# Kernel optimization log

Measured on AMD Instinct MI355X. Metric: run time of the kernel, lower is better.

## Reference

```python
import jax, jax.numpy as jnp
import numpy as np

B, T, V, D, H = 64, 256, 16, 64, 256  # batch, time, n_vars, d_inp, hidden


def setup_inputs() -> dict:
    key = jax.random.key(0)
    ks = jax.random.split(key, 20)
    s = 0.02
    inp = {
        "x": jax.random.normal(ks[0], (B, T, V, D), dtype=jnp.float32),
        # weight GRN: inp = V*D, hidden = H, out = V (skip linear present since V*D != V)
        "w_fc1_w": jax.random.normal(ks[1], (V * D, H), jnp.float32) * s,
        "w_fc1_b": jnp.zeros((H,), jnp.float32),
        "w_fc2_w": jax.random.normal(ks[2], (H, V), jnp.float32) * s,
        "w_fc2_b": jnp.zeros((V,), jnp.float32),
        "w_gate_w": jax.random.normal(ks[3], (V, V), jnp.float32) * s,
        "w_gate_b": jnp.zeros((V,), jnp.float32),
        "w_skip_w": jax.random.normal(ks[4], (V * D, V), jnp.float32) * s,
        "w_skip_b": jnp.zeros((V,), jnp.float32),
        # per-variable GRNs stacked over V: inp = D, hidden = H, out = H (skip since D != H)
        "v_fc1_w": jax.random.normal(ks[5], (V, D, H), jnp.float32) * s,
        "v_fc1_b": jnp.zeros((V, H), jnp.float32),
        "v_fc2_w": jax.random.normal(ks[6], (V, H, H), jnp.float32) * s,
        "v_fc2_b": jnp.zeros((V, H), jnp.float32),
        "v_gate_w": jax.random.normal(ks[7], (V, H, H), jnp.float32) * s,
        "v_gate_b": jnp.zeros((V, H), jnp.float32),
        "v_skip_w": jax.random.normal(ks[8], (V, D, H), jnp.float32) * s,
        "v_skip_b": jnp.zeros((V, H), jnp.float32),
    }
    return inp


def reference(x, w_fc1_w, w_fc1_b, w_fc2_w, w_fc2_b, w_gate_w, w_gate_b,
              w_skip_w, w_skip_b, v_fc1_w, v_fc1_b, v_fc2_w, v_fc2_b,
              v_gate_w, v_gate_b, v_skip_w, v_skip_b):
    # dropout is identity at inference
    Bx, Tx, Vx, Dx = x.shape
    flat = x.reshape(Bx, Tx, Vx * Dx)  # [B,T,V*D]

    # --- weight GRN: (V*D) -> V ---
    h = jax.nn.elu(flat @ w_fc1_w + w_fc1_b)          # [B,T,H]
    y = h @ w_fc2_w + w_fc2_b                          # [B,T,V]
    gate = jax.nn.sigmoid(y @ w_gate_w + w_gate_b)     # [B,T,V]
    res = flat @ w_skip_w + w_skip_b                   # [B,T,V]
    w = jax.nn.softmax(res + gate * y, axis=-1)        # [B,T,V]

    # --- per-variable GRNs, batched over V: D -> H ---
    hv = jax.nn.elu(jnp.einsum('btvd,vdh->btvh', x, v_fc1_w) + v_fc1_b)        # [B,T,V,H]
    yv = jnp.einsum('btvh,vhk->btvk', hv, v_fc2_w) + v_fc2_b                   # [B,T,V,H]
    gv = jax.nn.sigmoid(jnp.einsum('btvk,vkm->btvm', yv, v_gate_w) + v_gate_b) # [B,T,V,H]
    rv = jnp.einsum('btvd,vdk->btvk', x, v_skip_w) + v_skip_b                  # [B,T,V,H]
    var_outs = rv + gv * yv                                                    # [B,T,V,H]

    # softmax-weighted sum over variables
    z = jnp.einsum('btv,btvh->bth', w, var_outs)       # [B,T,H]
    return z
```

## Files before the change

### kernel.cpp

```cpp
#include <hip/hip_runtime.h>

typedef unsigned short u16;
typedef unsigned int   u32;
typedef __bf16 bf16x8 __attribute__((ext_vector_type(8)));
typedef u16    u16x8  __attribute__((ext_vector_type(8)));
typedef float  f32x4  __attribute__((ext_vector_type(4)));

#define DI static __device__ __forceinline__

DI float b2f(u16 u){ union { u32 i; float f; } c; c.i = ((u32)u) << 16; return c.f; }
DI u16 f2b(float f){ union { float f; u32 i; } c; c.f = f; u32 i = c.i;
                     return (u16)((i + 0x7FFFu + ((i >> 16) & 1u)) >> 16); }
DI float eluf(float x){ return x > 0.f ? x : (__expf(x) - 1.f); }
DI float sigf(float x){ return 1.f / (1.f + __expf(-x)); }
DI f32x4 mfma16(bf16x8 a, bf16x8 b, f32x4 c){
  return __builtin_amdgcn_mfma_f32_16x16x32_bf16(a, b, c, 0, 0, 0);
}
DI bf16x8 ldb(const u16* p){ return *(const bf16x8*)p; }

__global__ __launch_bounds__(256) void k_pack_x(
    const float* __restrict__ x, u16* __restrict__ pX)
{
  __shared__ u16 sX[16 * 1032];
  const int t  = threadIdx.x;
  const int rb = blockIdx.x;
  const float* xp = x + (size_t)rb * 16384;
  #pragma unroll
  for (int it = 0; it < 16; it++){
    float4 v4 = *(const float4*)&xp[it * 1024 + t * 4];
    u16x8 tmp;
    tmp[0] = f2b(v4.x); tmp[1] = f2b(v4.y); tmp[2] = f2b(v4.z); tmp[3] = f2b(v4.w);
    uint2 pk; pk.x = (u32)tmp[0] | ((u32)tmp[1] << 16); pk.y = (u32)tmp[2] | ((u32)tmp[3] << 16);
    *(uint2*)&sX[it * 1032 + t * 4] = pk;
  }
  __syncthreads();
  u16* dst = pX + (size_t)rb * 16384;
  #pragma unroll
  for (int u = 0; u < 8; u++){
    int c = u * 256 + t;
    int kc = c >> 6, lane = c & 63, ln = lane & 15, q = lane >> 4;
    u16x8 v = *(const u16x8*)&sX[ln * 1032 + kc * 32 + q * 8];
    *(uint4*)&dst[kc * 512 + lane * 8] = __builtin_bit_cast(uint4, v);
  }
}

__global__ __launch_bounds__(256) void k_pack_w(
    const float* __restrict__ wfc1, const float* __restrict__ wskip,
    const float* __restrict__ vfc1, const float* __restrict__ vfc2,
    const float* __restrict__ vgate, const float* __restrict__ vskip,
    u16* __restrict__ pW1, u16* __restrict__ pF1, u16* __restrict__ pSk,
    u16* __restrict__ pF2, u16* __restrict__ pGa)
{
  const int g = blockIdx.x * 256 + threadIdx.x;
  float v8[8];
  u16* dst;
  if (g < 34816){
    int idx = g, lane = idx & 63, kc = (idx >> 6) & 31, nb = idx >> 11;
    int ln = lane & 15, q = lane >> 4;
    #pragma unroll
    for (int j = 0; j < 8; j++){
      int k = kc * 32 + q * 8 + j;
      v8[j] = (nb < 16) ? wfc1[(size_t)k * 256 + nb * 16 + ln]
                        : wskip[(size_t)k * 16 + ln];
    }
    dst = pW1 + (size_t)idx * 8;
  } else if (g < 67584){
    int idx = g - 34816, lane = idx & 63, kc = (idx >> 6) & 1, nb = (idx >> 7) & 15, v = idx >> 11;
    int ln = lane & 15, q = lane >> 4;
    #pragma unroll
    for (int j = 0; j < 8; j++){
      int k = kc * 32 + q * 8 + j;
      v8[j] = vfc1[((size_t)v * 64 + k) * 256 + nb * 16 + ln];
    }
    dst = pF1 + (size_t)idx * 8;
  } else if (g < 100352){
    int idx = g - 67584, lane = idx & 63, kc = (idx >> 6) & 1, nb = (idx >> 7) & 15, v = idx >> 11;
    int ln = lane & 15, q = lane >> 4;
    #pragma unroll
    for (int j = 0; j < 8; j++){
      int k = kc * 32 + q * 8 + j;
      v8[j] = vskip[((size_t)v * 64 + k) * 256 + nb * 16 + ln];
    }
    dst = pSk + (size_t)idx * 8;
  } else if (g < 231424){
    int idx = g - 100352, lane = idx & 63, kc = (idx >> 6) & 7, nb = (idx >> 9) & 15, v = idx >> 13;
    int ln = lane & 15, q = lane >> 4;
    #pragma unroll
    for (int j = 0; j < 8; j++){
      int k = kc * 32 + q * 8 + j;
      v8[j] = vfc2[((size_t)v * 256 + k) * 256 + nb * 16 + ln];
    }
    dst = pF2 + (size_t)idx * 8;
  } else {
    int idx = g - 231424, lane = idx & 63, kc = (idx >> 6) & 7, nb = (idx >> 9) & 15, v = idx >> 13;
    int ln = lane & 15, q = lane >> 4;
    #pragma unroll
    for (int j = 0; j < 8; j++){
      int k = kc * 32 + q * 8 + j;
      v8[j] = vgate[((size_t)v * 256 + k) * 256 + nb * 16 + ln];
    }
    dst = pGa + (size_t)idx * 8;
  }
  u16x8 t;
  #pragma unroll
  for (int j = 0; j < 8; j++) t[j] = f2b(v8[j]);
  *(uint4*)dst = __builtin_bit_cast(uint4, t);
}

__global__ __launch_bounds__(512, 4) void k_weight_grn(
    const u16* __restrict__ pX, const u16* __restrict__ pW1,
    const float* __restrict__ b1, const float* __restrict__ W2, const float* __restrict__ b2,
    const float* __restrict__ Wg, const float* __restrict__ bg, const float* __restrict__ bs,
    float* __restrict__ w_out)
{
  __shared__ u16 sH[32 * 264];
  __shared__ float sR[32 * 16];
  __shared__ float sY[32 * 16];
  __shared__ float sG[32 * 16];
  __shared__ float sW2f[256 * 16];
  __shared__ float sWgf[256];

  const int tid  = threadIdx.x;
  const int lane = tid & 63;
  const int wid  = tid >> 6;
  const int ln   = lane & 15;
  const int q    = lane >> 4;
  const int row0 = blockIdx.x * 32;
  const int nb0  = wid * 2;
  const int ncnt = (wid == 7) ? 3 : 2;

  #pragma unroll
  for (int u = 0; u < 2; u++)
    *(float4*)&sW2f[tid * 8 + u * 4] = *(const float4*)&W2[tid * 8 + u * 4];
  if (tid < 256) sWgf[tid] = Wg[tid];

  f32x4 acc[2][3];
  #pragma unroll
  for (int mb = 0; mb < 2; mb++)
    #pragma unroll
    for (int i = 0; i < 3; i++){ acc[mb][i][0]=0.f; acc[mb][i][1]=0.f; acc[mb][i][2]=0.f; acc[mb][i][3]=0.f; }

  for (int kc = 0; kc < 32; kc++){
    bf16x8 a[2];
    #pragma unroll
    for (int mb = 0; mb < 2; mb++)
      a[mb] = ldb(&pX[((size_t)(blockIdx.x * 2 + mb) * 32 + kc) * 512 + lane * 8]);
    #pragma unroll
    for (int i = 0; i < 3; i++){
      if (i < ncnt){
        bf16x8 b = ldb(&pW1[(size_t)((nb0 + i) * 32 + kc) * 512 + lane * 8]);
        #pragma unroll
        for (int mb = 0; mb < 2; mb++) acc[mb][i] = mfma16(a[mb], b, acc[mb][i]);
      }
    }
  }

  #pragma unroll
  for (int i = 0; i < 3; i++){
    if (i < ncnt){
      int nb = nb0 + i;
      int col = nb * 16 + ln;
      float vb = (nb < 16) ? b1[col] : bs[ln];
      #pragma unroll
      for (int mb = 0; mb < 2; mb++){
        #pragma unroll
        for (int r = 0; r < 4; r++){
          int lr = mb * 16 + q * 4 + r;
          float v = acc[mb][i][r] + vb;
          if (nb < 16) sH[lr * 264 + col] = f2b(eluf(v));
          else         sR[lr * 16 + ln] = v;
        }
      }
    }
  }
  __syncthreads();

  {
    int r = tid >> 4, j = tid & 15;
    float a0 = b2[j];
    #pragma unroll 4
    for (int kb = 0; kb < 32; kb++){
      u16x8 h8 = *(const u16x8*)&sH[r * 264 + kb * 8];
      #pragma unroll
      for (int u = 0; u < 8; u++)
        a0 += b2f(h8[u]) * sW2f[(kb * 8 + u) * 16 + j];
    }
    sY[r * 16 + j] = a0;
  }
  __syncthreads();

  {
    int r = tid >> 4, j = tid & 15;
    float g0 = bg[j];
    #pragma unroll
    for (int k = 0; k < 16; k++)
      g0 += sY[r * 16 + k] * sWgf[k * 16 + j];
    sG[r * 16 + j] = sigf(g0);
  }
  __syncthreads();

  if (tid < 32){
    int r = tid;
    float l[16]; float m = -1e30f;
    #pragma unroll
    for (int j = 0; j < 16; j++){
      float v = sR[r * 16 + j] + sG[r * 16 + j] * sY[r * 16 + j];
      l[j] = v; m = fmaxf(m, v);
    }
    float s = 0.f;
    #pragma unroll
    for (int j = 0; j < 16; j++){ l[j] = __expf(l[j] - m); s += l[j]; }
    float inv = 1.f / s;
    #pragma unroll
    for (int j = 0; j < 16; j++) w_out[(size_t)(row0 + r) * 16 + j] = l[j] * inv;
  }
}

__global__ __launch_bounds__(512, 4) void k_var_grn(
    const u16* __restrict__ pX,
    const u16* __restrict__ pF1, const u16* __restrict__ pSk,
    const u16* __restrict__ pF2, const u16* __restrict__ pGa,
    const float* __restrict__ b1, const float* __restrict__ b2,
    const float* __restrict__ bg, const float* __restrict__ bs,
    const float* __restrict__ w_in, float* __restrict__ out)
{
  __shared__ u16 sHh[32 * 264];
  __shared__ u16 sHy[32 * 264];
  __shared__ float sWt[32 * 16];

  const int tid  = threadIdx.x;
  const int lane = tid & 63;
  const int wid  = tid >> 6;
  const int ln   = lane & 15;
  const int q    = lane >> 4;
  const int row0 = blockIdx.x * 32;
  const int rb0  = blockIdx.x * 2;
  const int nb0  = wid * 2;

  sWt[tid] = w_in[(size_t)row0 * 16 + tid];
  __syncthreads();

  f32x4 z[2][2];
  #pragma unroll
  for (int mb = 0; mb < 2; mb++)
    #pragma unroll
    for (int i = 0; i < 2; i++){ z[mb][i][0]=0.f; z[mb][i][1]=0.f; z[mb][i][2]=0.f; z[mb][i][3]=0.f; }

  #pragma unroll 1
  for (int v = 0; v < 16; v++){
    bf16x8 a0[2], a1[2];
    #pragma unroll
    for (int mb = 0; mb < 2; mb++){
      const u16* xp = &pX[((size_t)(rb0 + mb) * 32 + v * 2) * 512 + lane * 8];
      a0[mb] = ldb(xp);
      a1[mb] = ldb(xp + 512);
    }
    float wv[2][4];
    #pragma unroll
    for (int mb = 0; mb < 2; mb++)
      #pragma unroll
      for (int r = 0; r < 4; r++) wv[mb][r] = sWt[(mb * 16 + q * 4 + r) * 16 + v];

    f32x4 hacc[2][2];
    #pragma unroll
    for (int mb = 0; mb < 2; mb++)
      #pragma unroll
      for (int i = 0; i < 2; i++){ hacc[mb][i][0]=0.f; hacc[mb][i][1]=0.f; hacc[mb][i][2]=0.f; hacc[mb][i][3]=0.f; }
    #pragma unroll
    for (int ks = 0; ks < 2; ks++){
      bf16x8 B0 = ldb(&pF1[(size_t)((v * 16 + nb0) * 2 + ks) * 512 + lane * 8]);
      bf16x8 B1 = ldb(&pF1[(size_t)((v * 16 + nb0 + 1) * 2 + ks) * 512 + lane * 8]);
      #pragma unroll
      for (int mb = 0; mb < 2; mb++){
        bf16x8 a = ks ? a1[mb] : a0[mb];
        hacc[mb][0] = mfma16(a, B0, hacc[mb][0]);
        hacc[mb][1] = mfma16(a, B1, hacc[mb][1]);
      }
    }
    #pragma unroll
    for (int i = 0; i < 2; i++){
      int col = (nb0 + i) * 16 + ln;
      float vb = b1[v * 256 + col];
      #pragma unroll
      for (int mb = 0; mb < 2; mb++)
        #pragma unroll
        for (int r = 0; r < 4; r++)
          sHh[(mb * 16 + q * 4 + r) * 264 + col] = f2b(eluf(hacc[mb][i][r] + vb));
    }

    f32x4 racc[2][2];
    #pragma unroll
    for (int mb = 0; mb < 2; mb++)
      #pragma unroll
      for (int i = 0; i < 2; i++){ racc[mb][i][0]=0.f; racc[mb][i][1]=0.f; racc[mb][i][2]=0.f; racc[mb][i][3]=0.f; }
    #pragma unroll
    for (int ks = 0; ks < 2; ks++){
      bf16x8 B0 = ldb(&pSk[(size_t)((v * 16 + nb0) * 2 + ks) * 512 + lane * 8]);
      bf16x8 B1 = ldb(&pSk[(size_t)((v * 16 + nb0 + 1) * 2 + ks) * 512 + lane * 8]);
      #pragma unroll
      for (int mb = 0; mb < 2; mb++){
        bf16x8 a = ks ? a1[mb] : a0[mb];
        racc[mb][0] = mfma16(a, B0, racc[mb][0]);
        racc[mb][1] = mfma16(a, B1, racc[mb][1]);
      }
    }
    #pragma unroll
    for (int i = 0; i < 2; i++){
      float vb = bs[v * 256 + (nb0 + i) * 16 + ln];
      #pragma unroll
      for (int mb = 0; mb < 2; mb++)
        #pragma unroll
        for (int r = 0; r < 4; r++) z[mb][i][r] += wv[mb][r] * (racc[mb][i][r] + vb);
    }
    __syncthreads();

    f32x4 yacc[2][2];
    #pragma unroll
    for (int mb = 0; mb < 2; mb++)
      #pragma unroll
      for (int i = 0; i < 2; i++){ yacc[mb][i][0]=0.f; yacc[mb][i][1]=0.f; yacc[mb][i][2]=0.f; yacc[mb][i][3]=0.f; }
    #pragma unroll
    for (int kc = 0; kc < 8; kc++){
      bf16x8 B0 = ldb(&pF2[(size_t)((v * 16 + nb0) * 8 + kc) * 512 + lane * 8]);
      bf16x8 B1 = ldb(&pF2[(size_t)((v * 16 + nb0 + 1) * 8 + kc) * 512 + lane * 8]);
      #pragma unroll
      for (int mb = 0; mb < 2; mb++){
        bf16x8 ah = *(const bf16x8*)&sHh[(mb * 16 + ln) * 264 + kc * 32 + q * 8];
        yacc[mb][0] = mfma16(ah, B0, yacc[mb][0]);
        yacc[mb][1] = mfma16(ah, B1, yacc[mb][1]);
      }
    }
    f32x4 ysave[2][2];
    #pragma unroll
    for (int i = 0; i < 2; i++){
      int col = (nb0 + i) * 16 + ln;
      float vb = b2[v * 256 + col];
      #pragma unroll
      for (int mb = 0; mb < 2; mb++)
        #pragma unroll
        for (int r = 0; r < 4; r++){
          float yy = yacc[mb][i][r] + vb;
          ysave[mb][i][r] = yy;
          sHy[(mb * 16 + q * 4 + r) * 264 + col] = f2b(yy);
        }
    }
    __syncthreads();

    f32x4 gacc[2][2];
    #pragma unroll
    for (int mb = 0; mb < 2; mb++)
      #pragma unroll
      for (int i = 0; i < 2; i++){ gacc[mb][i][0]=0.f; gacc[mb][i][1]=0.f; gacc[mb][i][2]=0.f; gacc[mb][i][3]=0.f; }
    #pragma unroll
    for (int kc = 0; kc < 8; kc++){
      bf16x8 B0 = ldb(&pGa[(size_t)((v * 16 + nb0) * 8 + kc) * 512 + lane * 8]);
      bf16x8 B1 = ldb(&pGa[(size_t)((v * 16 + nb0 + 1) * 8 + kc) * 512 + lane * 8]);
      #pragma unroll
      for (int mb = 0; mb < 2; mb++){
        bf16x8 ah = *(const bf16x8*)&sHy[(mb * 16 + ln) * 264 + kc * 32 + q * 8];
        gacc[mb][0] = mfma16(ah, B0, gacc[mb][0]);
        gacc[mb][1] = mfma16(ah, B1, gacc[mb][1]);
      }
    }
    #pragma unroll
    for (int i = 0; i < 2; i++){
      float vb = bg[v * 256 + (nb0 + i) * 16 + ln];
      #pragma unroll
      for (int mb = 0; mb < 2; mb++)
        #pragma unroll
        for (int r = 0; r < 4; r++)
          z[mb][i][r] += wv[mb][r] * sigf(gacc[mb][i][r] + vb) * ysave[mb][i][r];
    }
  }

  #pragma unroll
  for (int i = 0; i < 2; i++){
    int col = (nb0 + i) * 16 + ln;
    #pragma unroll
    for (int mb = 0; mb < 2; mb++)
      #pragma unroll
      for (int r = 0; r < 4; r++)
        out[(size_t)(row0 + mb * 16 + q * 4 + r) * 256 + col] = z[mb][i][r];
  }
}

extern "C" void kernel_launch(void* const* d_in, const int* in_sizes, int n_in,
                              void* d_out, int out_size, void* d_ws, size_t ws_size,
                              hipStream_t stream)
{
  const float* x     = (const float*)d_in[0];
  const float* wfc1w = (const float*)d_in[1];
  const float* wfc1b = (const float*)d_in[2];
  const float* wfc2w = (const float*)d_in[3];
  const float* wfc2b = (const float*)d_in[4];
  const float* wgw   = (const float*)d_in[5];
  const float* wgb   = (const float*)d_in[6];
  const float* wsw   = (const float*)d_in[7];
  const float* wsb   = (const float*)d_in[8];
  const float* vfc1w = (const float*)d_in[9];
  const float* vfc1b = (const float*)d_in[10];
  const float* vfc2w = (const float*)d_in[11];
  const float* vfc2b = (const float*)d_in[12];
  const float* vgw   = (const float*)d_in[13];
  const float* vgb   = (const float*)d_in[14];
  const float* vsw   = (const float*)d_in[15];
  const float* vsb   = (const float*)d_in[16];

  u16* ws   = (u16*)d_ws;
  u16* pX   = ws;
  u16* pW1  = pX + 16777216;
  u16* pF1  = pW1 + 278528;
  u16* pSk  = pF1 + 262144;
  u16* pF2  = pSk + 262144;
  u16* pGa  = pF2 + 1048576;
  float* w_ws = (float*)(pGa + 1048576);

  k_pack_w<<<dim3(1416), dim3(256), 0, stream>>>(
      wfc1w, wsw, vfc1w, vfc2w, vgw, vsw, pW1, pF1, pSk, pF2, pGa);

  k_pack_x<<<dim3(1024), dim3(256), 0, stream>>>(x, pX);

  k_weight_grn<<<dim3(512), dim3(512), 0, stream>>>(
      pX, pW1, wfc1b, wfc2w, wfc2b, wgw, wgb, wsb, w_ws);

  k_var_grn<<<dim3(512), dim3(512), 0, stream>>>(
      pX, pF1, pSk, pF2, pGa, vfc1b, vfc2b, vgb, vsb, w_ws, (float*)d_out);
}
```

Before: 361.0 us.

## Merge pack kernels and software-prefetch per-variable weight fragments in var GRN

Fuses the x-pack and weight-pack kernels into a single launch whose block index selects the role, removing one kernel launch and letting both run concurrently. In the per-variable GRN loop, weight fragments for the next variable (fc1, skip) and for the later stages (fc2, gate) are loaded into registers ahead of use and interleaved with MFMA work, so global load latency overlaps compute. The skip GEMM is reordered to run first. This raises register pressure, which may lower occupancy or cause spills under the 512-thread launch bound.

```diff
diff --git a/kernel.cpp b/kernel.cpp
--- a/kernel.cpp
+++ b/kernel.cpp
@@ -18,40 +18,38 @@
 }
 DI bf16x8 ldb(const u16* p){ return *(const bf16x8*)p; }
 
-__global__ __launch_bounds__(256) void k_pack_x(
-    const float* __restrict__ x, u16* __restrict__ pX)
-{
-  __shared__ u16 sX[16 * 1032];
-  const int t  = threadIdx.x;
-  const int rb = blockIdx.x;
-  const float* xp = x + (size_t)rb * 16384;
-  #pragma unroll
-  for (int it = 0; it < 16; it++){
-    float4 v4 = *(const float4*)&xp[it * 1024 + t * 4];
-    u16x8 tmp;
-    tmp[0] = f2b(v4.x); tmp[1] = f2b(v4.y); tmp[2] = f2b(v4.z); tmp[3] = f2b(v4.w);
-    uint2 pk; pk.x = (u32)tmp[0] | ((u32)tmp[1] << 16); pk.y = (u32)tmp[2] | ((u32)tmp[3] << 16);
-    *(uint2*)&sX[it * 1032 + t * 4] = pk;
-  }
-  __syncthreads();
-  u16* dst = pX + (size_t)rb * 16384;
-  #pragma unroll
-  for (int u = 0; u < 8; u++){
-    int c = u * 256 + t;
-    int kc = c >> 6, lane = c & 63, ln = lane & 15, q = lane >> 4;
-    u16x8 v = *(const u16x8*)&sX[ln * 1032 + kc * 32 + q * 8];
-    *(uint4*)&dst[kc * 512 + lane * 8] = __builtin_bit_cast(uint4, v);
-  }
-}
-
-__global__ __launch_bounds__(256) void k_pack_w(
+__global__ __launch_bounds__(256) void k_pack(
+    const float* __restrict__ x,
     const float* __restrict__ wfc1, const float* __restrict__ wskip,
     const float* __restrict__ vfc1, const float* __restrict__ vfc2,
     const float* __restrict__ vgate, const float* __restrict__ vskip,
-    u16* __restrict__ pW1, u16* __restrict__ pF1, u16* __restrict__ pSk,
-    u16* __restrict__ pF2, u16* __restrict__ pGa)
+    u16* __restrict__ pX, u16* __restrict__ pW1, u16* __restrict__ pF1,
+    u16* __restrict__ pSk, u16* __restrict__ pF2, u16* __restrict__ pGa)
 {
-  const int g = blockIdx.x * 256 + threadIdx.x;
+  __shared__ u16 sX[16 * 1032];
+  const int t = threadIdx.x;
+  if (blockIdx.x < 1024){
+    const int rb = blockIdx.x;
+    const float* xp = x + (size_t)rb * 16384;
+    #pragma unroll
+    for (int it = 0; it < 16; it++){
+      float4 v4 = *(const float4*)&xp[it * 1024 + t * 4];
+      u16 t0 = f2b(v4.x), t1 = f2b(v4.y), t2 = f2b(v4.z), t3 = f2b(v4.w);
+      uint2 pk; pk.x = (u32)t0 | ((u32)t1 << 16); pk.y = (u32)t2 | ((u32)t3 << 16);
+      *(uint2*)&sX[it * 1032 + t * 4] = pk;
+    }
+    __syncthreads();
+    u16* dst = pX + (size_t)rb * 16384;
+    #pragma unroll
+    for (int u = 0; u < 8; u++){
+      int c = u * 256 + t;
+      int kc = c >> 6, lane = c & 63, ln = lane & 15, q = lane >> 4;
+      u16x8 v = *(const u16x8*)&sX[ln * 1032 + kc * 32 + q * 8];
+      *(uint4*)&dst[kc * 512 + lane * 8] = __builtin_bit_cast(uint4, v);
+    }
+    return;
+  }
+  const int g = (blockIdx.x - 1024) * 256 + t;
   float v8[8];
   u16* dst;
   if (g < 34816){
@@ -101,10 +99,10 @@
     }
     dst = pGa + (size_t)idx * 8;
   }
-  u16x8 t;
-  #pragma unroll
-  for (int j = 0; j < 8; j++) t[j] = f2b(v8[j]);
-  *(uint4*)dst = __builtin_bit_cast(uint4, t);
+  u16x8 tv;
+  #pragma unroll
+  for (int j = 0; j < 8; j++) tv[j] = f2b(v8[j]);
+  *(uint4*)dst = __builtin_bit_cast(uint4, tv);
 }
 
 __global__ __launch_bounds__(512, 4) void k_weight_grn(
@@ -246,6 +244,15 @@
     #pragma unroll
     for (int i = 0; i < 2; i++){ z[mb][i][0]=0.f; z[mb][i][1]=0.f; z[mb][i][2]=0.f; z[mb][i][3]=0.f; }
 
+  bf16x8 Bf1[2][2], Bsk[2][2];
+  #pragma unroll
+  for (int ks = 0; ks < 2; ks++)
+    #pragma unroll
+    for (int i = 0; i < 2; i++){
+      Bf1[i][ks] = ldb(&pF1[(size_t)((nb0 + i) * 2 + ks) * 512 + lane * 8]);
+      Bsk[i][ks] = ldb(&pSk[(size_t)((nb0 + i) * 2 + ks) * 512 + lane * 8]);
+    }
+
   #pragma unroll 1
   for (int v = 0; v < 16; v++){
     bf16x8 a0[2], a1[2];
@@ -261,22 +268,55 @@
       #pragma unroll
       for (int r = 0; r < 4; r++) wv[mb][r] = sWt[(mb * 16 + q * 4 + r) * 16 + v];
 
+    f32x4 racc[2][2];
+    #pragma unroll
+    for (int mb = 0; mb < 2; mb++)
+      #pragma unroll
+      for (int i = 0; i < 2; i++){ racc[mb][i][0]=0.f; racc[mb][i][1]=0.f; racc[mb][i][2]=0.f; racc[mb][i][3]=0.f; }
+    #pragma unroll
+    for (int ks = 0; ks < 2; ks++)
+      #pragma unroll
+      for (int mb = 0; mb < 2; mb++){
+        bf16x8 a = ks ? a1[mb] : a0[mb];
+        racc[mb][0] = mfma16(a, Bsk[0][ks], racc[mb][0]);
+        racc[mb][1] = mfma16(a, Bsk[1][ks], racc[mb][1]);
+      }
+    #pragma unroll
+    for (int i = 0; i < 2; i++){
+      float vb = bs[v * 256 + (nb0 + i) * 16 + ln];
+      #pragma unroll
+      for (int mb = 0; mb < 2; mb++)
+        #pragma unroll
+        for (int r = 0; r < 4; r++) z[mb][i][r] += wv[mb][r] * (racc[mb][i][r] + vb);
+    }
+
+    bf16x8 Bf2[2][8];
+    #pragma unroll
+    for (int kc = 0; kc < 4; kc++){
+      Bf2[0][kc] = ldb(&pF2[(size_t)((v * 16 + nb0) * 8 + kc) * 512 + lane * 8]);
+      Bf2[1][kc] = ldb(&pF2[(size_t)((v * 16 + nb0 + 1) * 8 + kc) * 512 + lane * 8]);
+    }
+
     f32x4 hacc[2][2];
     #pragma unroll
     for (int mb = 0; mb < 2; mb++)
       #pragma unroll
       for (int i = 0; i < 2; i++){ hacc[mb][i][0]=0.f; hacc[mb][i][1]=0.f; hacc[mb][i][2]=0.f; hacc[mb][i][3]=0.f; }
     #pragma unroll
-    for (int ks = 0; ks < 2; ks++){
-      bf16x8 B0 = ldb(&pF1[(size_t)((v * 16 + nb0) * 2 + ks) * 512 + lane * 8]);
-      bf16x8 B1 = ldb(&pF1[(size_t)((v * 16 + nb0 + 1) * 2 + ks) * 512 + lane * 8]);
+    for (int ks = 0; ks < 2; ks++)
       #pragma unroll
       for (int mb = 0; mb < 2; mb++){
         bf16x8 a = ks ? a1[mb] : a0[mb];
-        hacc[mb][0] = mfma16(a, B0, hacc[mb][0]);
-        hacc[mb][1] = mfma16(a, B1, hacc[mb][1]);
-      }
-    }
+        hacc[mb][0] = mfma16(a, Bf1[0][ks], hacc[mb][0]);
+        hacc[mb][1] = mfma16(a, Bf1[1][ks], hacc[mb][1]);
+      }
+
+    #pragma unroll
+    for (int kc = 4; kc < 8; kc++){
+      Bf2[0][kc] = ldb(&pF2[(size_t)((v * 16 + nb0) * 8 + kc) * 512 + lane * 8]);
+      Bf2[1][kc] = ldb(&pF2[(size_t)((v * 16 + nb0 + 1) * 8 + kc) * 512 + lane * 8]);
+    }
+
     #pragma unroll
     for (int i = 0; i < 2; i++){
       int col = (nb0 + i) * 16 + ln;
@@ -287,31 +327,6 @@
         for (int r = 0; r < 4; r++)
           sHh[(mb * 16 + q * 4 + r) * 264 + col] = f2b(eluf(hacc[mb][i][r] + vb));
     }
-
-    f32x4 racc[2][2];
-    #pragma unroll
-    for (int mb = 0; mb < 2; mb++)
-      #pragma unroll
-      for (int i = 0; i < 2; i++){ racc[mb][i][0]=0.f; racc[mb][i][1]=0.f; racc[mb][i][2]=0.f; racc[mb][i][3]=0.f; }
-    #pragma unroll
-    for (int ks = 0; ks < 2; ks++){
-      bf16x8 B0 = ldb(&pSk[(size_t)((v * 16 + nb0) * 2 + ks) * 512 + lane * 8]);
-      bf16x8 B1 = ldb(&pSk[(size_t)((v * 16 + nb0 + 1) * 2 + ks) * 512 + lane * 8]);
-      #pragma unroll
-      for (int mb = 0; mb < 2; mb++){
-        bf16x8 a = ks ? a1[mb] : a0[mb];
-        racc[mb][0] = mfma16(a, B0, racc[mb][0]);
-        racc[mb][1] = mfma16(a, B1, racc[mb][1]);
-      }
-    }
-    #pragma unroll
-    for (int i = 0; i < 2; i++){
-      float vb = bs[v * 256 + (nb0 + i) * 16 + ln];
-      #pragma unroll
-      for (int mb = 0; mb < 2; mb++)
-        #pragma unroll
-        for (int r = 0; r < 4; r++) z[mb][i][r] += wv[mb][r] * (racc[mb][i][r] + vb);
-    }
     __syncthreads();
 
     f32x4 yacc[2][2];
@@ -320,16 +335,21 @@
       #pragma unroll
       for (int i = 0; i < 2; i++){ yacc[mb][i][0]=0.f; yacc[mb][i][1]=0.f; yacc[mb][i][2]=0.f; yacc[mb][i][3]=0.f; }
     #pragma unroll
+    for (int kc = 0; kc < 8; kc++)
+      #pragma unroll
+      for (int mb = 0; mb < 2; mb++){
+        bf16x8 ah = *(const bf16x8*)&sHh[(mb * 16 + ln) * 264 + kc * 32 + q * 8];
+        yacc[mb][0] = mfma16(ah, Bf2[0][kc], yacc[mb][0]);
+        yacc[mb][1] = mfma16(ah, Bf2[1][kc], yacc[mb][1]);
+      }
+
+    bf16x8 Bga[2][8];
+    #pragma unroll
     for (int kc = 0; kc < 8; kc++){
-      bf16x8 B0 = ldb(&pF2[(size_t)((v * 16 + nb0) * 8 + kc) * 512 + lane * 8]);
-      bf16x8 B1 = ldb(&pF2[(size_t)((v * 16 + nb0 + 1) * 8 + kc) * 512 + lane * 8]);
-      #pragma unroll
-      for (int mb = 0; mb < 2; mb++){
-        bf16x8 ah = *(const bf16x8*)&sHh[(mb * 16 + ln) * 264 + kc * 32 + q * 8];
-        yacc[mb][0] = mfma16(ah, B0, yacc[mb][0]);
-        yacc[mb][1] = mfma16(ah, B1, yacc[mb][1]);
-      }
-    }
+      Bga[0][kc] = ldb(&pGa[(size_t)((v * 16 + nb0) * 8 + kc) * 512 + lane * 8]);
+      Bga[1][kc] = ldb(&pGa[(size_t)((v * 16 + nb0 + 1) * 8 + kc) * 512 + lane * 8]);
+    }
+
     f32x4 ysave[2][2];
     #pragma unroll
     for (int i = 0; i < 2; i++){
@@ -352,16 +372,41 @@
       #pragma unroll
       for (int i = 0; i < 2; i++){ gacc[mb][i][0]=0.f; gacc[mb][i][1]=0.f; gacc[mb][i][2]=0.f; gacc[mb][i][3]=0.f; }
     #pragma unroll
-    for (int kc = 0; kc < 8; kc++){
-      bf16x8 B0 = ldb(&pGa[(size_t)((v * 16 + nb0) * 8 + kc) * 512 + lane * 8]);
-      bf16x8 B1 = ldb(&pGa[(size_t)((v * 16 + nb0 + 1) * 8 + kc) * 512 + lane * 8]);
+    for (int kc = 0; kc < 4; kc++)
       #pragma unroll
       for (int mb = 0; mb < 2; mb++){
         bf16x8 ah = *(const bf16x8*)&sHy[(mb * 16 + ln) * 264 + kc * 32 + q * 8];
-        gacc[mb][0] = mfma16(ah, B0, gacc[mb][0]);
-        gacc[mb][1] = mfma16(ah, B1, gacc[mb][1]);
-      }
-    }
+        gacc[mb][0] = mfma16(ah, Bga[0][kc], gacc[mb][0]);
+        gacc[mb][1] = mfma16(ah, Bga[1][kc], gacc[mb][1]);
+      }
+
+    {
+      int vn = (v + 1) & 15;
+      #pragma unroll
+      for (int ks = 0; ks < 2; ks++)
+        #pragma unroll
+        for (int i = 0; i < 2; i++)
+          Bf1[i][ks] = ldb(&pF1[(size_t)(((vn * 16) + nb0 + i) * 2 + ks) * 512 + lane * 8]);
+    }
+
+    #pragma unroll
+    for (int kc = 4; kc < 8; kc++)
+      #pragma unroll
+      for (int mb = 0; mb < 2; mb++){
+        bf16x8 ah = *(const bf16x8*)&sHy[(mb * 16 + ln) * 264 + kc * 32 + q * 8];
+        gacc[mb][0] = mfma16(ah, Bga[0][kc], gacc[mb][0]);
+        gacc[mb][1] = mfma16(ah, Bga[1][kc], gacc[mb][1]);
+      }
+
+    {
+      int vn = (v + 1) & 15;
+      #pragma unroll
+      for (int ks = 0; ks < 2; ks++)
+        #pragma unroll
+        for (int i = 0; i < 2; i++)
+          Bsk[i][ks] = ldb(&pSk[(size_t)(((vn * 16) + nb0 + i) * 2 + ks) * 512 + lane * 8]);
+    }
+
     #pragma unroll
     for (int i = 0; i < 2; i++){
       float vb = bg[v * 256 + (nb0 + i) * 16 + ln];
@@ -415,10 +460,8 @@
   u16* pGa  = pF2 + 1048576;
   float* w_ws = (float*)(pGa + 1048576);
 
-  k_pack_w<<<dim3(1416), dim3(256), 0, stream>>>(
-      wfc1w, wsw, vfc1w, vfc2w, vgw, vsw, pW1, pF1, pSk, pF2, pGa);
-
-  k_pack_x<<<dim3(1024), dim3(256), 0, stream>>>(x, pX);
+  k_pack<<<dim3(2440), dim3(256), 0, stream>>>(
+      x, wfc1w, wsw, vfc1w, vfc2w, vgw, vsw, pX, pW1, pF1, pSk, pF2, pGa);
 
   k_weight_grn<<<dim3(512), dim3(512), 0, stream>>>(
       pX, pW1, wfc1b, wfc2w, wfc2b, wgw, wgb, wsb, w_ws);
```

Result: slower. 495.3 us (+37.2%).

## Fuse weight GRN into variable GRN kernel and merge packing kernels

Applied to the files above, without the earlier changes.

The x-packing and weight-packing kernels become one launch that picks its role by block index. The weight GRN, which computes the softmax variable weights, now runs in the prologue of the variable GRN kernel, so the weights stay in shared memory instead of going through a global buffer. Shared memory is overlaid so that buffers from the weight-GRN phase are reused by the later phase. The float-to-bf16 rounding now uses the native bf16 conversion. This removes two launches and a global round trip, but puts the serial weight-GRN work at the front of each fused block.

```diff
diff --git a/kernel.cpp b/kernel.cpp
--- a/kernel.cpp
+++ b/kernel.cpp
@@ -9,8 +9,7 @@
 #define DI static __device__ __forceinline__
 
 DI float b2f(u16 u){ union { u32 i; float f; } c; c.i = ((u32)u) << 16; return c.f; }
-DI u16 f2b(float f){ union { float f; u32 i; } c; c.f = f; u32 i = c.i;
-                     return (u16)((i + 0x7FFFu + ((i >> 16) & 1u)) >> 16); }
+DI u16 f2b(float f){ return __builtin_bit_cast(u16, (__bf16)f); }
 DI float eluf(float x){ return x > 0.f ? x : (__expf(x) - 1.f); }
 DI float sigf(float x){ return 1.f / (1.f + __expf(-x)); }
 DI f32x4 mfma16(bf16x8 a, bf16x8 b, f32x4 c){
@@ -18,40 +17,38 @@
 }
 DI bf16x8 ldb(const u16* p){ return *(const bf16x8*)p; }
 
-__global__ __launch_bounds__(256) void k_pack_x(
-    const float* __restrict__ x, u16* __restrict__ pX)
-{
-  __shared__ u16 sX[16 * 1032];
-  const int t  = threadIdx.x;
-  const int rb = blockIdx.x;
-  const float* xp = x + (size_t)rb * 16384;
-  #pragma unroll
-  for (int it = 0; it < 16; it++){
-    float4 v4 = *(const float4*)&xp[it * 1024 + t * 4];
-    u16x8 tmp;
-    tmp[0] = f2b(v4.x); tmp[1] = f2b(v4.y); tmp[2] = f2b(v4.z); tmp[3] = f2b(v4.w);
-    uint2 pk; pk.x = (u32)tmp[0] | ((u32)tmp[1] << 16); pk.y = (u32)tmp[2] | ((u32)tmp[3] << 16);
-    *(uint2*)&sX[it * 1032 + t * 4] = pk;
-  }
-  __syncthreads();
-  u16* dst = pX + (size_t)rb * 16384;
-  #pragma unroll
-  for (int u = 0; u < 8; u++){
-    int c = u * 256 + t;
-    int kc = c >> 6, lane = c & 63, ln = lane & 15, q = lane >> 4;
-    u16x8 v = *(const u16x8*)&sX[ln * 1032 + kc * 32 + q * 8];
-    *(uint4*)&dst[kc * 512 + lane * 8] = __builtin_bit_cast(uint4, v);
-  }
-}
-
-__global__ __launch_bounds__(256) void k_pack_w(
+__global__ __launch_bounds__(256) void k_pack(
+    const float* __restrict__ x,
     const float* __restrict__ wfc1, const float* __restrict__ wskip,
     const float* __restrict__ vfc1, const float* __restrict__ vfc2,
     const float* __restrict__ vgate, const float* __restrict__ vskip,
-    u16* __restrict__ pW1, u16* __restrict__ pF1, u16* __restrict__ pSk,
-    u16* __restrict__ pF2, u16* __restrict__ pGa)
+    u16* __restrict__ pX, u16* __restrict__ pW1, u16* __restrict__ pF1,
+    u16* __restrict__ pSk, u16* __restrict__ pF2, u16* __restrict__ pGa)
 {
-  const int g = blockIdx.x * 256 + threadIdx.x;
+  __shared__ u16 sX[16 * 1032];
+  const int t = threadIdx.x;
+  if (blockIdx.x < 1024){
+    const int rb = blockIdx.x;
+    const float* xp = x + (size_t)rb * 16384;
+    #pragma unroll
+    for (int it = 0; it < 16; it++){
+      float4 v4 = *(const float4*)&xp[it * 1024 + t * 4];
+      u16 t0 = f2b(v4.x), t1 = f2b(v4.y), t2 = f2b(v4.z), t3 = f2b(v4.w);
+      uint2 pk; pk.x = (u32)t0 | ((u32)t1 << 16); pk.y = (u32)t2 | ((u32)t3 << 16);
+      *(uint2*)&sX[it * 1032 + t * 4] = pk;
+    }
+    __syncthreads();
+    u16* dst = pX + (size_t)rb * 16384;
+    #pragma unroll
+    for (int u = 0; u < 8; u++){
+      int c = u * 256 + t;
+      int kc = c >> 6, lane = c & 63, ln = lane & 15, q = lane >> 4;
+      u16x8 v = *(const u16x8*)&sX[ln * 1032 + kc * 32 + q * 8];
+      *(uint4*)&dst[kc * 512 + lane * 8] = __builtin_bit_cast(uint4, v);
+    }
+    return;
+  }
+  const int g = (blockIdx.x - 1024) * 256 + t;
   float v8[8];
   u16* dst;
   if (g < 34816){
@@ -101,132 +98,31 @@
     }
     dst = pGa + (size_t)idx * 8;
   }
-  u16x8 t;
+  u16x8 tv;
   #pragma unroll
-  for (int j = 0; j < 8; j++) t[j] = f2b(v8[j]);
-  *(uint4*)dst = __builtin_bit_cast(uint4, t);
+  for (int j = 0; j < 8; j++) tv[j] = f2b(v8[j]);
+  *(uint4*)dst = __builtin_bit_cast(uint4, tv);
 }
 
-__global__ __launch_bounds__(512, 4) void k_weight_grn(
+__global__ __launch_bounds__(512, 4) void k_fused(
     const u16* __restrict__ pX, const u16* __restrict__ pW1,
-    const float* __restrict__ b1, const float* __restrict__ W2, const float* __restrict__ b2,
-    const float* __restrict__ Wg, const float* __restrict__ bg, const float* __restrict__ bs,
-    float* __restrict__ w_out)
-{
-  __shared__ u16 sH[32 * 264];
-  __shared__ float sR[32 * 16];
-  __shared__ float sY[32 * 16];
-  __shared__ float sG[32 * 16];
-  __shared__ float sW2f[256 * 16];
-  __shared__ float sWgf[256];
-
-  const int tid  = threadIdx.x;
-  const int lane = tid & 63;
-  const int wid  = tid >> 6;
-  const int ln   = lane & 15;
-  const int q    = lane >> 4;
-  const int row0 = blockIdx.x * 32;
-  const int nb0  = wid * 2;
-  const int ncnt = (wid == 7) ? 3 : 2;
-
-  #pragma unroll
-  for (int u = 0; u < 2; u++)
-    *(float4*)&sW2f[tid * 8 + u * 4] = *(const float4*)&W2[tid * 8 + u * 4];
-  if (tid < 256) sWgf[tid] = Wg[tid];
-
-  f32x4 acc[2][3];
-  #pragma unroll
-  for (int mb = 0; mb < 2; mb++)
-    #pragma unroll
-    for (int i = 0; i < 3; i++){ acc[mb][i][0]=0.f; acc[mb][i][1]=0.f; acc[mb][i][2]=0.f; acc[mb][i][3]=0.f; }
-
-  for (int kc = 0; kc < 32; kc++){
-    bf16x8 a[2];
-    #pragma unroll
-    for (int mb = 0; mb < 2; mb++)
-      a[mb] = ldb(&pX[((size_t)(blockIdx.x * 2 + mb) * 32 + kc) * 512 + lane * 8]);
-    #pragma unroll
-    for (int i = 0; i < 3; i++){
-      if (i < ncnt){
-        bf16x8 b = ldb(&pW1[(size_t)((nb0 + i) * 32 + kc) * 512 + lane * 8]);
-        #pragma unroll
-        for (int mb = 0; mb < 2; mb++) acc[mb][i] = mfma16(a[mb], b, acc[mb][i]);
-      }
-    }
-  }
-
-  #pragma unroll
-  for (int i = 0; i < 3; i++){
-    if (i < ncnt){
-      int nb = nb0 + i;
-      int col = nb * 16 + ln;
-      float vb = (nb < 16) ? b1[col] : bs[ln];
-      #pragma unroll
-      for (int mb = 0; mb < 2; mb++){
-        #pragma unroll
-        for (int r = 0; r < 4; r++){
-          int lr = mb * 16 + q * 4 + r;
-          float v = acc[mb][i][r] + vb;
-          if (nb < 16) sH[lr * 264 + col] = f2b(eluf(v));
-          else         sR[lr * 16 + ln] = v;
-        }
-      }
-    }
-  }
-  __syncthreads();
-
-  {
-    int r = tid >> 4, j = tid & 15;
-    float a0 = b2[j];
-    #pragma unroll 4
-    for (int kb = 0; kb < 32; kb++){
-      u16x8 h8 = *(const u16x8*)&sH[r * 264 + kb * 8];
-      #pragma unroll
-      for (int u = 0; u < 8; u++)
-        a0 += b2f(h8[u]) * sW2f[(kb * 8 + u) * 16 + j];
-    }
-    sY[r * 16 + j] = a0;
-  }
-  __syncthreads();
-
-  {
-    int r = tid >> 4, j = tid & 15;
-    float g0 = bg[j];
-    #pragma unroll
-    for (int k = 0; k < 16; k++)
-      g0 += sY[r * 16 + k] * sWgf[k * 16 + j];
-    sG[r * 16 + j] = sigf(g0);
-  }
-  __syncthreads();
-
-  if (tid < 32){
-    int r = tid;
-    float l[16]; float m = -1e30f;
-    #pragma unroll
-    for (int j = 0; j < 16; j++){
-      float v = sR[r * 16 + j] + sG[r * 16 + j] * sY[r * 16 + j];
-      l[j] = v; m = fmaxf(m, v);
-    }
-    float s = 0.f;
-    #pragma unroll
-    for (int j = 0; j < 16; j++){ l[j] = __expf(l[j] - m); s += l[j]; }
-    float inv = 1.f / s;
-    #pragma unroll
-    for (int j = 0; j < 16; j++) w_out[(size_t)(row0 + r) * 16 + j] = l[j] * inv;
-  }
-}
-
-__global__ __launch_bounds__(512, 4) void k_var_grn(
-    const u16* __restrict__ pX,
     const u16* __restrict__ pF1, const u16* __restrict__ pSk,
     const u16* __restrict__ pF2, const u16* __restrict__ pGa,
+    const float* __restrict__ wb1, const float* __restrict__ W2,
+    const float* __restrict__ wb2, const float* __restrict__ Wg,
+    const float* __restrict__ wbg, const float* __restrict__ wbs,
     const float* __restrict__ b1, const float* __restrict__ b2,
     const float* __restrict__ bg, const float* __restrict__ bs,
-    const float* __restrict__ w_in, float* __restrict__ out)
+    float* __restrict__ out)
 {
-  __shared__ u16 sHh[32 * 264];
-  __shared__ u16 sHy[32 * 264];
-  __shared__ float sWt[32 * 16];
+  __shared__ __align__(16) char smem[40960];
+  u16*   sHh  = (u16*)smem;
+  u16*   sHy  = (u16*)(smem + 16896);
+  float* sW2f = (float*)(smem + 16896);
+  float* sWt  = (float*)(smem + 33792);
+  float* sR   = (float*)(smem + 35840);
+  float* sY   = (float*)(smem + 37888);
+  float* sWgf = (float*)(smem + 39936);
 
   const int tid  = threadIdx.x;
   const int lane = tid & 63;
@@ -237,8 +133,95 @@
   const int rb0  = blockIdx.x * 2;
   const int nb0  = wid * 2;
 
-  sWt[tid] = w_in[(size_t)row0 * 16 + tid];
-  __syncthreads();
+  {
+    const int ncnt = (wid == 7) ? 3 : 2;
+    #pragma unroll
+    for (int u = 0; u < 2; u++)
+      *(float4*)&sW2f[tid * 8 + u * 4] = *(const float4*)&W2[tid * 8 + u * 4];
+    if (tid < 256) sWgf[tid] = Wg[tid];
+
+    f32x4 acc[2][3];
+    #pragma unroll
+    for (int mb = 0; mb < 2; mb++)
+      #pragma unroll
+      for (int i = 0; i < 3; i++){ acc[mb][i][0]=0.f; acc[mb][i][1]=0.f; acc[mb][i][2]=0.f; acc[mb][i][3]=0.f; }
+
+    for (int kc = 0; kc < 32; kc++){
+      bf16x8 a[2];
+      #pragma unroll
+      for (int mb = 0; mb < 2; mb++)
+        a[mb] = ldb(&pX[((size_t)(rb0 + mb) * 32 + kc) * 512 + lane * 8]);
+      #pragma unroll
+      for (int i = 0; i < 3; i++){
+        if (i < ncnt){
+          bf16x8 b = ldb(&pW1[(size_t)((nb0 + i) * 32 + kc) * 512 + lane * 8]);
+          #pragma unroll
+          for (int mb = 0; mb < 2; mb++) acc[mb][i] = mfma16(a[mb], b, acc[mb][i]);
+        }
+      }
+    }
+
+    #pragma unroll
+    for (int i = 0; i < 3; i++){
+      if (i < ncnt){
+        int nb = nb0 + i;
+        int col = nb * 16 + ln;
+        float vb = (nb < 16) ? wb1[col] : wbs[ln];
+        #pragma unroll
+        for (int mb = 0; mb < 2; mb++){
+          #pragma unroll
+          for (int r = 0; r < 4; r++){
+            int lr = mb * 16 + q * 4 + r;
+            float v = acc[mb][i][r] + vb;
+            if (nb < 16) sHh[lr * 264 + col] = f2b(eluf(v));
+            else         sR[lr * 16 + ln] = v;
+          }
+        }
+      }
+    }
+    __syncthreads();
+
+    {
+      int r = tid >> 4, j = tid & 15;
+      float a0 = wb2[j];
+      #pragma unroll 4
+      for (int kb = 0; kb < 32; kb++){
+        u16x8 h8 = *(const u16x8*)&sHh[r * 264 + kb * 8];
+        #pragma unroll
+        for (int u = 0; u < 8; u++)
+          a0 += b2f(h8[u]) * sW2f[(kb * 8 + u) * 16 + j];
+      }
+      sY[r * 16 + j] = a0;
+    }
+    __syncthreads();
+
+    {
+      int r = tid >> 4, j = tid & 15;
+      float g0 = wbg[j];
+      #pragma unroll
+      for (int k = 0; k < 16; k++)
+        g0 += sY[r * 16 + k] * sWgf[k * 16 + j];
+      sWt[r * 16 + j] = sigf(g0);
+    }
+    __syncthreads();
+
+    if (tid < 32){
+      int r = tid;
+      float l[16]; float m = -1e30f;
+      #pragma unroll
+      for (int j = 0; j < 16; j++){
+        float v = sR[r * 16 + j] + sWt[r * 16 + j] * sY[r * 16 + j];
+        l[j] = v; m = fmaxf(m, v);
+      }
+      float s = 0.f;
+      #pragma unroll
+      for (int j = 0; j < 16; j++){ l[j] = __expf(l[j] - m); s += l[j]; }
+      float inv = 1.f / s;
+      #pragma unroll
+      for (int j = 0; j < 16; j++) sWt[r * 16 + j] = l[j] * inv;
+    }
+    __syncthreads();
+  }
 
   f32x4 z[2][2];
   #pragma unroll
@@ -413,16 +396,12 @@
   u16* pSk  = pF1 + 262144;
   u16* pF2  = pSk + 262144;
   u16* pGa  = pF2 + 1048576;
-  float* w_ws = (float*)(pGa + 1048576);
-
-  k_pack_w<<<dim3(1416), dim3(256), 0, stream>>>(
-      wfc1w, wsw, vfc1w, vfc2w, vgw, vsw, pW1, pF1, pSk, pF2, pGa);
-
-  k_pack_x<<<dim3(1024), dim3(256), 0, stream>>>(x, pX);
-
-  k_weight_grn<<<dim3(512), dim3(512), 0, stream>>>(
-      pX, pW1, wfc1b, wfc2w, wfc2b, wgw, wgb, wsb, w_ws);
-
-  k_var_grn<<<dim3(512), dim3(512), 0, stream>>>(
-      pX, pF1, pSk, pF2, pGa, vfc1b, vfc2b, vgb, vsb, w_ws, (float*)d_out);
+
+  k_pack<<<dim3(2440), dim3(256), 0, stream>>>(
+      x, wfc1w, wsw, vfc1w, vfc2w, vgw, vsw, pX, pW1, pF1, pSk, pF2, pGa);
+
+  k_fused<<<dim3(512), dim3(512), 0, stream>>>(
+      pX, pW1, pF1, pSk, pF2, pGa,
+      wfc1b, wfc2w, wfc2b, wgw, wgb, wsb,
+      vfc1b, vfc2b, vgb, vsb, (float*)d_out);
 }
```

Measured after the change: 368.3 us. Within noise of the previous version (+2.0%).

## Fuse x bf16 packing into weight GRN and tile weight packing through LDS

Applied to the files above, without the earlier changes.

Removes the separate x packing kernel. The weight GRN kernel now reads fp32 x directly, converts it to bf16 MFMA fragments in registers, and has wave 0 write the packed tile for the var-GRN kernel. The weight pack kernel is restructured into 32x256 tiles staged through shared memory with coalesced float4 reads, replacing strided scalar gathers. bf16 conversion uses the native cast. This saves one launch and a full extra read/write pass over x, but the fused GEMM now loads fp32 x (twice the bytes) directly in its inner loop.

```diff
diff --git a/kernel.cpp b/kernel.cpp
--- a/kernel.cpp
+++ b/kernel.cpp
@@ -9,38 +9,38 @@
 #define DI static __device__ __forceinline__
 
 DI float b2f(u16 u){ union { u32 i; float f; } c; c.i = ((u32)u) << 16; return c.f; }
-DI u16 f2b(float f){ union { float f; u32 i; } c; c.f = f; u32 i = c.i;
-                     return (u16)((i + 0x7FFFu + ((i >> 16) & 1u)) >> 16); }
+DI u16 f2b(float f){ return __builtin_bit_cast(u16, (__bf16)f); }
 DI float eluf(float x){ return x > 0.f ? x : (__expf(x) - 1.f); }
 DI float sigf(float x){ return 1.f / (1.f + __expf(-x)); }
 DI f32x4 mfma16(bf16x8 a, bf16x8 b, f32x4 c){
   return __builtin_amdgcn_mfma_f32_16x16x32_bf16(a, b, c, 0, 0, 0);
 }
 DI bf16x8 ldb(const u16* p){ return *(const bf16x8*)p; }
-
-__global__ __launch_bounds__(256) void k_pack_x(
-    const float* __restrict__ x, u16* __restrict__ pX)
-{
-  __shared__ u16 sX[16 * 1032];
-  const int t  = threadIdx.x;
-  const int rb = blockIdx.x;
-  const float* xp = x + (size_t)rb * 16384;
-  #pragma unroll
-  for (int it = 0; it < 16; it++){
-    float4 v4 = *(const float4*)&xp[it * 1024 + t * 4];
-    u16x8 tmp;
-    tmp[0] = f2b(v4.x); tmp[1] = f2b(v4.y); tmp[2] = f2b(v4.z); tmp[3] = f2b(v4.w);
-    uint2 pk; pk.x = (u32)tmp[0] | ((u32)tmp[1] << 16); pk.y = (u32)tmp[2] | ((u32)tmp[3] << 16);
-    *(uint2*)&sX[it * 1032 + t * 4] = pk;
-  }
-  __syncthreads();
-  u16* dst = pX + (size_t)rb * 16384;
+DI bf16x8 cvt8f(float4 a, float4 b){
+  u16x8 t;
+  t[0]=f2b(a.x); t[1]=f2b(a.y); t[2]=f2b(a.z); t[3]=f2b(a.w);
+  t[4]=f2b(b.x); t[5]=f2b(b.y); t[6]=f2b(b.z); t[7]=f2b(b.w);
+  return __builtin_bit_cast(bf16x8, t);
+}
+
+DI void stage_tile(const float* __restrict__ W, int t, u16* sT){
   #pragma unroll
   for (int u = 0; u < 8; u++){
-    int c = u * 256 + t;
-    int kc = c >> 6, lane = c & 63, ln = lane & 15, q = lane >> 4;
-    u16x8 v = *(const u16x8*)&sX[ln * 1032 + kc * 32 + q * 8];
-    *(uint4*)&dst[kc * 512 + lane * 8] = __builtin_bit_cast(uint4, v);
+    int c = u * 256 + t, row = c >> 6, colf = (c & 63) * 4;
+    float4 v4 = *(const float4*)&W[row * 256 + colf];
+    u16 a = f2b(v4.x), b = f2b(v4.y), cc = f2b(v4.z), d = f2b(v4.w);
+    uint2 pk; pk.x = (u32)a | ((u32)b << 16); pk.y = (u32)cc | ((u32)d << 16);
+    *(uint2*)&sT[row * 260 + colf] = pk;
+  }
+}
+DI void emit_tile(const u16* sT, int t, u16* dstbase, int kc, int KC){
+  #pragma unroll
+  for (int u = 0; u < 4; u++){
+    int g = u * 256 + t, nb = g >> 6, lane = g & 63, ln = lane & 15, q = lane >> 4;
+    u16x8 tv;
+    #pragma unroll
+    for (int j = 0; j < 8; j++) tv[j] = sT[(q * 8 + j) * 260 + nb * 16 + ln];
+    *(uint4*)&dstbase[((size_t)(nb * KC + kc)) * 512 + lane * 8] = __builtin_bit_cast(uint4, tv);
   }
 }
 
@@ -48,70 +48,63 @@
     const float* __restrict__ wfc1, const float* __restrict__ wskip,
     const float* __restrict__ vfc1, const float* __restrict__ vfc2,
     const float* __restrict__ vgate, const float* __restrict__ vskip,
-    u16* __restrict__ pW1, u16* __restrict__ pF1, u16* __restrict__ pSk,
-    u16* __restrict__ pF2, u16* __restrict__ pGa)
+    u16* __restrict__ pW1, u16* __restrict__ pF1,
+    u16* __restrict__ pSk, u16* __restrict__ pF2, u16* __restrict__ pGa)
 {
-  const int g = blockIdx.x * 256 + threadIdx.x;
-  float v8[8];
-  u16* dst;
-  if (g < 34816){
-    int idx = g, lane = idx & 63, kc = (idx >> 6) & 31, nb = idx >> 11;
-    int ln = lane & 15, q = lane >> 4;
-    #pragma unroll
-    for (int j = 0; j < 8; j++){
-      int k = kc * 32 + q * 8 + j;
-      v8[j] = (nb < 16) ? wfc1[(size_t)k * 256 + nb * 16 + ln]
-                        : wskip[(size_t)k * 16 + ln];
-    }
-    dst = pW1 + (size_t)idx * 8;
-  } else if (g < 67584){
-    int idx = g - 34816, lane = idx & 63, kc = (idx >> 6) & 1, nb = (idx >> 7) & 15, v = idx >> 11;
-    int ln = lane & 15, q = lane >> 4;
-    #pragma unroll
-    for (int j = 0; j < 8; j++){
-      int k = kc * 32 + q * 8 + j;
-      v8[j] = vfc1[((size_t)v * 64 + k) * 256 + nb * 16 + ln];
-    }
-    dst = pF1 + (size_t)idx * 8;
-  } else if (g < 100352){
-    int idx = g - 67584, lane = idx & 63, kc = (idx >> 6) & 1, nb = (idx >> 7) & 15, v = idx >> 11;
-    int ln = lane & 15, q = lane >> 4;
-    #pragma unroll
-    for (int j = 0; j < 8; j++){
-      int k = kc * 32 + q * 8 + j;
-      v8[j] = vskip[((size_t)v * 64 + k) * 256 + nb * 16 + ln];
-    }
-    dst = pSk + (size_t)idx * 8;
-  } else if (g < 231424){
-    int idx = g - 100352, lane = idx & 63, kc = (idx >> 6) & 7, nb = (idx >> 9) & 15, v = idx >> 13;
-    int ln = lane & 15, q = lane >> 4;
-    #pragma unroll
-    for (int j = 0; j < 8; j++){
-      int k = kc * 32 + q * 8 + j;
-      v8[j] = vfc2[((size_t)v * 256 + k) * 256 + nb * 16 + ln];
-    }
-    dst = pF2 + (size_t)idx * 8;
+  __shared__ u16 sX[32 * 260];
+  const int t  = threadIdx.x;
+  const int wb = blockIdx.x;
+  if (wb == 32){
+    __shared__ u16 sS[1024 * 16];
+    #pragma unroll
+    for (int u = 0; u < 64; u++){
+      int c = u * 256 + t, row = c >> 2, colf = (c & 3) * 4;
+      float4 v4 = *(const float4*)&wskip[row * 16 + colf];
+      u16 a = f2b(v4.x), b = f2b(v4.y), cc = f2b(v4.z), d = f2b(v4.w);
+      uint2 pk; pk.x = (u32)a | ((u32)b << 16); pk.y = (u32)cc | ((u32)d << 16);
+      *(uint2*)&sS[row * 16 + colf] = pk;
+    }
+    __syncthreads();
+    #pragma unroll
+    for (int u = 0; u < 8; u++){
+      int g = u * 256 + t, kc = g >> 6, lane = g & 63, ln = lane & 15, q = lane >> 4;
+      u16x8 tv;
+      #pragma unroll
+      for (int j = 0; j < 8; j++) tv[j] = sS[(kc * 32 + q * 8 + j) * 16 + ln];
+      *(uint4*)&pW1[((size_t)(16 * 32 + kc)) * 512 + lane * 8] = __builtin_bit_cast(uint4, tv);
+    }
+    return;
+  }
+  const float* src; u16* dstbase; int kc, KC;
+  if (wb < 32){
+    kc = wb; KC = 32; src = wfc1 + (size_t)kc * 32 * 256; dstbase = pW1;
+  } else if (wb < 65){
+    int idx = wb - 33, v = idx >> 1, ks = idx & 1;
+    kc = ks; KC = 2; src = vfc1 + ((size_t)v * 64 + ks * 32) * 256;
+    dstbase = pF1 + (size_t)v * 32 * 512;
+  } else if (wb < 97){
+    int idx = wb - 65, v = idx >> 1, ks = idx & 1;
+    kc = ks; KC = 2; src = vskip + ((size_t)v * 64 + ks * 32) * 256;
+    dstbase = pSk + (size_t)v * 32 * 512;
+  } else if (wb < 225){
+    int idx = wb - 97, v = idx >> 3, kk = idx & 7;
+    kc = kk; KC = 8; src = vfc2 + ((size_t)v * 256 + kk * 32) * 256;
+    dstbase = pF2 + (size_t)v * 128 * 512;
   } else {
-    int idx = g - 231424, lane = idx & 63, kc = (idx >> 6) & 7, nb = (idx >> 9) & 15, v = idx >> 13;
-    int ln = lane & 15, q = lane >> 4;
-    #pragma unroll
-    for (int j = 0; j < 8; j++){
-      int k = kc * 32 + q * 8 + j;
-      v8[j] = vgate[((size_t)v * 256 + k) * 256 + nb * 16 + ln];
-    }
-    dst = pGa + (size_t)idx * 8;
-  }
-  u16x8 t;
-  #pragma unroll
-  for (int j = 0; j < 8; j++) t[j] = f2b(v8[j]);
-  *(uint4*)dst = __builtin_bit_cast(uint4, t);
+    int idx = wb - 225, v = idx >> 3, kk = idx & 7;
+    kc = kk; KC = 8; src = vgate + ((size_t)v * 256 + kk * 32) * 256;
+    dstbase = pGa + (size_t)v * 128 * 512;
+  }
+  stage_tile(src, t, sX);
+  __syncthreads();
+  emit_tile(sX, t, dstbase, kc, KC);
 }
 
 __global__ __launch_bounds__(512, 4) void k_weight_grn(
-    const u16* __restrict__ pX, const u16* __restrict__ pW1,
+    const float* __restrict__ x, const u16* __restrict__ pW1,
     const float* __restrict__ b1, const float* __restrict__ W2, const float* __restrict__ b2,
     const float* __restrict__ Wg, const float* __restrict__ bg, const float* __restrict__ bs,
-    float* __restrict__ w_out)
+    float* __restrict__ w_out, u16* __restrict__ pX)
 {
   __shared__ u16 sH[32 * 264];
   __shared__ float sR[32 * 16];
@@ -126,6 +119,7 @@
   const int ln   = lane & 15;
   const int q    = lane >> 4;
   const int row0 = blockIdx.x * 32;
+  const int rb0  = blockIdx.x * 2;
   const int nb0  = wid * 2;
   const int ncnt = (wid == 7) ? 3 : 2;
 
@@ -143,8 +137,16 @@
   for (int kc = 0; kc < 32; kc++){
     bf16x8 a[2];
     #pragma unroll
-    for (int mb = 0; mb < 2; mb++)
-      a[mb] = ldb(&pX[((size_t)(blockIdx.x * 2 + mb) * 32 + kc) * 512 + lane * 8]);
+    for (int mb = 0; mb < 2; mb++){
+      const float* xp = &x[(size_t)(row0 + mb * 16 + ln) * 1024 + kc * 32 + q * 8];
+      a[mb] = cvt8f(*(const float4*)xp, *(const float4*)(xp + 4));
+    }
+    if (wid == 0){
+      #pragma unroll
+      for (int mb = 0; mb < 2; mb++)
+        *(uint4*)&pX[((size_t)(rb0 + mb) * 32 + kc) * 512 + lane * 8] =
+            __builtin_bit_cast(uint4, a[mb]);
+    }
     #pragma unroll
     for (int i = 0; i < 3; i++){
       if (i < ncnt){
@@ -415,13 +417,11 @@
   u16* pGa  = pF2 + 1048576;
   float* w_ws = (float*)(pGa + 1048576);
 
-  k_pack_w<<<dim3(1416), dim3(256), 0, stream>>>(
+  k_pack_w<<<dim3(353), dim3(256), 0, stream>>>(
       wfc1w, wsw, vfc1w, vfc2w, vgw, vsw, pW1, pF1, pSk, pF2, pGa);
 
-  k_pack_x<<<dim3(1024), dim3(256), 0, stream>>>(x, pX);
-
   k_weight_grn<<<dim3(512), dim3(512), 0, stream>>>(
-      pX, pW1, wfc1b, wfc2w, wfc2b, wgw, wgb, wsb, w_ws);
+      x, pW1, wfc1b, wfc2w, wfc2b, wgw, wgb, wsb, w_ws, pX);
 
   k_var_grn<<<dim3(512), dim3(512), 0, stream>>>(
       pX, pF1, pSk, pF2, pGa, vfc1b, vfc2b, vgb, vsb, w_ws, (float*)d_out);
```

Measured after the change: 406.3 us. 1.13x slower.
